# Performance work log

Hardware: AMD Instinct MI355X
Metric: run time of the kernel (lower is better)

The kernel has to match this reference:

```python
import jax, jax.numpy as jnp
import numpy as np

EPS = 1e-5

def _bn(h, gamma, beta):
    # BatchNorm1d in training mode: per-channel stats over the batch dim (L=1)
    m = jnp.mean(h, axis=0)
    v = jnp.var(h, axis=0)  # biased variance, as torch uses for normalization
    return gamma * (h - m) * jax.lax.rsqrt(v + EPS) + beta

def setup_inputs() -> dict:
    key = jax.random.key(0)
    ks = jax.random.split(key, 8)
    vocab, emb = 8192, 512
    inter = (vocab + emb) // 2  # 4352
    N = 8192
    x_t = jax.random.randint(ks[0], (N,), 0, vocab, dtype=jnp.int64)
    W1 = jax.random.normal(ks[1], (inter, vocab), dtype=jnp.float32) * 0.02
    b1 = jax.random.normal(ks[2], (inter,), dtype=jnp.float32) * 0.02
    g1 = jnp.ones((inter,), dtype=jnp.float32)
    beta1 = jnp.zeros((inter,), dtype=jnp.float32)
    W2 = jax.random.normal(ks[3], (emb, inter), dtype=jnp.float32) * 0.02
    b2 = jax.random.normal(ks[4], (emb,), dtype=jnp.float32) * 0.02
    g2 = jnp.ones((emb,), dtype=jnp.float32)
    beta2 = jnp.zeros((emb,), dtype=jnp.float32)
    return {"x_t": x_t, "W1": W1, "b1": b1, "g1": g1, "beta1": beta1,
            "W2": W2, "b2": b2, "g2": g2, "beta2": beta2}

def reference(x_t, W1, b1, g1, beta1, W2, b2, g2, beta2):
    # one_hot(x_t) @ Conv1d(k=1) weight == gather of W1 columns (same math, no dense one-hot)
    h1 = W1.T[x_t] + b1                      # [N, inter]
    h1 = jax.nn.gelu(_bn(h1, g1, beta1), approximate=False)
    h2 = h1 @ W2.T + b2                      # [N, emb]
    out = jax.nn.gelu(_bn(h2, g2, beta2), approximate=False)
    return out
```

## Files before the change

### kernel.cpp

```cpp
#include <hip/hip_runtime.h>
#include <hip/hip_bf16.h>
#include <math.h>

typedef __attribute__((ext_vector_type(8))) short short8;
typedef __attribute__((ext_vector_type(4))) float f32x4;

#define VOCAB 8192
#define NSAMP 8192
#define INTER 4352
#define EMB   512

#define OFF_CNT    0
#define OFF_A1     32768
#define OFF_M1     50176
#define OFF_A2     67584
#define OFF_M2     69632
#define OFF_PS1B   71680
#define OFF_PS2B   1120256
#define OFF_W2B    2168832
#define OFF_HACT   6625280
#define OFF_HPART  77928448
#define PART_BYTES 16777216ULL

__device__ __forceinline__ float gelu_exact(float x) {
    return 0.5f * x * (1.0f + erff(x * 0.70710678118654752f));
}
__device__ __forceinline__ unsigned short f2bf(float x) {
    __hip_bfloat16 b = __float2bfloat16(x);
    return *reinterpret_cast<unsigned short*>(&b);
}
__device__ __forceinline__ void async16(const unsigned short* g, unsigned short* l) {
    __builtin_amdgcn_global_load_lds(
        (const __attribute__((address_space(1))) void*)g,
        (__attribute__((address_space(3))) void*)l, 16, 0, 0);
}

__global__ void k_zero_cnt(int* cnt) {
    cnt[blockIdx.x * 256 + threadIdx.x] = 0;
}
__global__ void k_hist(const int* __restrict__ xt, int* __restrict__ cnt) {
    int n = blockIdx.x * 256 + threadIdx.x;
    atomicAdd(&cnt[xt[n]], 1);
}

__global__ __launch_bounds__(256) void k_stats1(const float* __restrict__ W1,
                                                const int* __restrict__ cnt,
                                                const float* __restrict__ g1,
                                                float* __restrict__ a1,
                                                float* __restrict__ m1) {
    const int t = threadIdx.x, lane = t & 63, w = t >> 6;
    const int row = blockIdx.x * 4 + w;
    const float* wr = W1 + (size_t)row * VOCAB;
    float s1 = 0.f, s2 = 0.f;
    #pragma unroll 8
    for (int it = 0; it < 32; ++it) {
        int v = it * 256 + lane * 4;
        float4 x = *(const float4*)(wr + v);
        int4 c = *(const int4*)(cnt + v);
        float cx = (float)c.x, cy = (float)c.y, cz = (float)c.z, cw = (float)c.w;
        s1 += cx * x.x + cy * x.y + cz * x.z + cw * x.w;
        s2 += cx * x.x * x.x + cy * x.y * x.y + cz * x.z * x.z + cw * x.w * x.w;
    }
    #pragma unroll
    for (int d = 1; d < 64; d <<= 1) {
        s1 += __shfl_xor(s1, d);
        s2 += __shfl_xor(s2, d);
    }
    if (lane == 0) {
        float m = s1 * (1.f / NSAMP);
        float var = s2 * (1.f / NSAMP) - m * m;
        a1[row] = g1[row] * rsqrtf(var + 1e-5f);
        m1[row] = m;
    }
}

__global__ __launch_bounds__(256) void k_build(const float* __restrict__ W1,
                                               const float* __restrict__ a1,
                                               const float* __restrict__ m1,
                                               const float* __restrict__ beta1,
                                               unsigned short* __restrict__ Hact) {
    const int i0 = blockIdx.x * 64;
    const int v0 = blockIdx.y * 256;
    const int t = threadIdx.x;
    const int c0 = (t & 15) * 4;
    const int vg = (t >> 4) * 4;
    float4 av = *(const float4*)(a1 + i0 + c0);
    float4 mv = *(const float4*)(m1 + i0 + c0);
    float4 bv = *(const float4*)(beta1 + i0 + c0);
    const float* ap = (const float*)&av;
    const float* mp = (const float*)&mv;
    const float* bp = (const float*)&bv;
    #pragma unroll
    for (int vi = 0; vi < 4; ++vi) {
        int vb = v0 + vi * 64 + vg;
        float wf[4][4];
        #pragma unroll
        for (int j = 0; j < 4; ++j)
            *(float4*)&wf[j][0] = *(const float4*)(W1 + (size_t)(i0 + c0 + j) * VOCAB + vb);
        #pragma unroll
        for (int k = 0; k < 4; ++k) {
            ushort4 o;
            o.x = f2bf(gelu_exact(ap[0] * (wf[0][k] - mp[0]) + bp[0]));
            o.y = f2bf(gelu_exact(ap[1] * (wf[1][k] - mp[1]) + bp[1]));
            o.z = f2bf(gelu_exact(ap[2] * (wf[2][k] - mp[2]) + bp[2]));
            o.w = f2bf(gelu_exact(ap[3] * (wf[3][k] - mp[3]) + bp[3]));
            *(ushort4*)&Hact[(size_t)(vb + k) * INTER + i0 + c0] = o;
        }
    }
}

__global__ void k_w2bf(const float* __restrict__ W2, unsigned short* __restrict__ W2b) {
    int idx = (blockIdx.x * 256 + threadIdx.x) * 4;
    float4 w = *(const float4*)(W2 + idx);
    ushort4 u;
    u.x = f2bf(w.x); u.y = f2bf(w.y); u.z = f2bf(w.z); u.w = f2bf(w.w);
    *(ushort4*)(W2b + idx) = u;
}

__global__ __launch_bounds__(512) void k_gemm(const unsigned short* __restrict__ A,
                                              const unsigned short* __restrict__ B,
                                              float* __restrict__ Cp, int kPer) {
    __shared__ __align__(16) unsigned short sA[128 * 64];
    __shared__ __align__(16) unsigned short sB[512 * 64];
    const int m0 = blockIdx.x * 128;
    const int kbeg = blockIdx.z * kPer;
    const int kend = kbeg + kPer;
    float* C = Cp + (size_t)blockIdx.z * NSAMP * EMB;
    const int t = threadIdx.x;
    const int lane = t & 63;
    const int wave = t >> 6;
    const int wr = wave >> 2, wc = wave & 3;
    const int mq = lane & 15, kq = lane >> 4;
    const int srow = lane >> 3;
    const int sgrp = lane & 7;
    const int scol = (sgrp ^ srow) * 8;
    const int swz = mq & 7;
    f32x4 acc[4][8];
    #pragma unroll
    for (int r = 0; r < 4; ++r)
        #pragma unroll
        for (int c = 0; c < 8; ++c) acc[r][c] = (f32x4){0.f, 0.f, 0.f, 0.f};
    for (int k0 = kbeg; k0 < kend; k0 += 64) {
        #pragma unroll
        for (int p = 0; p < 2; ++p) {
            int r0 = wave * 16 + p * 8;
            async16(A + (size_t)(m0 + r0 + srow) * INTER + k0 + scol, &sA[r0 * 64]);
        }
        #pragma unroll
        for (int p = 0; p < 8; ++p) {
            int r0 = wave * 64 + p * 8;
            async16(B + (size_t)(r0 + srow) * INTER + k0 + scol, &sB[r0 * 64]);
        }
        __syncthreads();
        #pragma unroll
        for (int kk = 0; kk < 64; kk += 32) {
            const int gbase = kq + (kk >> 3);
            short8 af[4], bf[8];
            #pragma unroll
            for (int r = 0; r < 4; ++r)
                af[r] = *(const short8*)&sA[(wr * 64 + r * 16 + mq) * 64 + ((gbase ^ swz) * 8)];
            #pragma unroll
            for (int c = 0; c < 8; ++c)
                bf[c] = *(const short8*)&sB[(wc * 128 + c * 16 + mq) * 64 + ((gbase ^ swz) * 8)];
            #pragma unroll
            for (int r = 0; r < 4; ++r)
                #pragma unroll
                for (int c = 0; c < 8; ++c)
                    acc[r][c] = __builtin_amdgcn_mfma_f32_16x16x32_bf16(af[r], bf[c], acc[r][c], 0, 0, 0);
        }
        __syncthreads();
    }
    #pragma unroll
    for (int r = 0; r < 4; ++r) {
        #pragma unroll
        for (int c = 0; c < 8; ++c) {
            int col = wc * 128 + c * 16 + mq;
            int rowb = m0 + wr * 64 + r * 16 + kq * 4;
            #pragma unroll
            for (int j = 0; j < 4; ++j)
                C[(size_t)(rowb + j) * EMB + col] = acc[r][c][j];
        }
    }
}

__global__ __launch_bounds__(256) void k_reduce(const float* hpart,
                                                const int* __restrict__ cnt,
                                                float* h2,
                                                float* __restrict__ ps1,
                                                float* __restrict__ ps2, int S) {
    __shared__ float4 b1[128], b2[128];
    const int v0 = blockIdx.x * 16;
    const int t = threadIdx.x;
    const int half = t >> 7;
    const int c4 = (t & 127) * 4;
    float4 acc1 = {0.f, 0.f, 0.f, 0.f}, acc2 = {0.f, 0.f, 0.f, 0.f};
    #pragma unroll
    for (int rp = 0; rp < 8; ++rp) {
        int r = v0 + rp * 2 + half;
        int cw_i = cnt[r];
        if (cw_i > 0) {
            size_t off = (size_t)r * EMB + c4;
            float4 h = *(const float4*)(hpart + off);
            for (int s = 1; s < S; ++s) {
                float4 hs = *(const float4*)(hpart + (size_t)s * NSAMP * EMB + off);
                h.x += hs.x; h.y += hs.y; h.z += hs.z; h.w += hs.w;
            }
            *(float4*)(h2 + off) = h;
            float w = (float)cw_i;
            acc1.x += w * h.x; acc1.y += w * h.y; acc1.z += w * h.z; acc1.w += w * h.w;
            acc2.x += w * h.x * h.x; acc2.y += w * h.y * h.y;
            acc2.z += w * h.z * h.z; acc2.w += w * h.w * h.w;
        }
    }
    if (half == 1) { b1[t & 127] = acc1; b2[t & 127] = acc2; }
    __syncthreads();
    if (half == 0) {
        float4 o1 = b1[t & 127], o2 = b2[t & 127];
        o1.x += acc1.x; o1.y += acc1.y; o1.z += acc1.z; o1.w += acc1.w;
        o2.x += acc2.x; o2.y += acc2.y; o2.z += acc2.z; o2.w += acc2.w;
        ps1[(size_t)(c4 + 0) * 512 + blockIdx.x] = o1.x;
        ps1[(size_t)(c4 + 1) * 512 + blockIdx.x] = o1.y;
        ps1[(size_t)(c4 + 2) * 512 + blockIdx.x] = o1.z;
        ps1[(size_t)(c4 + 3) * 512 + blockIdx.x] = o1.w;
        ps2[(size_t)(c4 + 0) * 512 + blockIdx.x] = o2.x;
        ps2[(size_t)(c4 + 1) * 512 + blockIdx.x] = o2.y;
        ps2[(size_t)(c4 + 2) * 512 + blockIdx.x] = o2.z;
        ps2[(size_t)(c4 + 3) * 512 + blockIdx.x] = o2.w;
    }
}

__global__ __launch_bounds__(256) void k_stats2f(const float* __restrict__ ps1,
                                                 const float* __restrict__ ps2,
                                                 const float* __restrict__ g2,
                                                 float* __restrict__ a2,
                                                 float* __restrict__ m2) {
    const int lane = threadIdx.x & 63;
    const int e = blockIdx.x * 4 + (threadIdx.x >> 6);
    float s1 = 0.f, s2 = 0.f;
    #pragma unroll
    for (int k = 0; k < 8; ++k) {
        s1 += ps1[(size_t)e * 512 + k * 64 + lane];
        s2 += ps2[(size_t)e * 512 + k * 64 + lane];
    }
    #pragma unroll
    for (int d = 1; d < 64; d <<= 1) {
        s1 += __shfl_xor(s1, d);
        s2 += __shfl_xor(s2, d);
    }
    if (lane == 0) {
        float m = s1 * (1.f / NSAMP);
        float var = s2 * (1.f / NSAMP) - m * m;
        a2[e] = g2[e] * rsqrtf(var + 1e-5f);
        m2[e] = m;
    }
}

__global__ __launch_bounds__(256) void k_final(const float* __restrict__ h2,
                                               const int* __restrict__ xt,
                                               const float* __restrict__ a2,
                                               const float* __restrict__ m2,
                                               const float* __restrict__ beta2,
                                               float* __restrict__ out) {
    const int t = threadIdx.x;
    const int n = blockIdx.x * 2 + (t >> 7);
    const int e = (t & 127) * 4;
    const int v = xt[n];
    float4 h = *(const float4*)(h2 + (size_t)v * EMB + e);
    float4 a = *(const float4*)(a2 + e);
    float4 m = *(const float4*)(m2 + e);
    float4 b = *(const float4*)(beta2 + e);
    float4 o;
    o.x = gelu_exact(a.x * (h.x - m.x) + b.x);
    o.y = gelu_exact(a.y * (h.y - m.y) + b.y);
    o.z = gelu_exact(a.z * (h.z - m.z) + b.z);
    o.w = gelu_exact(a.w * (h.w - m.w) + b.w);
    *(float4*)(out + (size_t)n * EMB + e) = o;
}

extern "C" void kernel_launch(void* const* d_in, const int* in_sizes, int n_in,
                              void* d_out, int out_size, void* d_ws, size_t ws_size,
                              hipStream_t stream) {
    const int* xt      = (const int*)d_in[0];
    const float* W1    = (const float*)d_in[1];
    const float* g1    = (const float*)d_in[3];
    const float* beta1 = (const float*)d_in[4];
    const float* W2    = (const float*)d_in[5];
    const float* g2    = (const float*)d_in[7];
    const float* beta2 = (const float*)d_in[8];
    float* out = (float*)d_out;

    char* ws = (char*)d_ws;
    int*   cnt  = (int*)  (ws + OFF_CNT);
    float* a1   = (float*)(ws + OFF_A1);
    float* m1   = (float*)(ws + OFF_M1);
    float* a2   = (float*)(ws + OFF_A2);
    float* m2   = (float*)(ws + OFF_M2);
    float* ps1b = (float*)(ws + OFF_PS1B);
    float* ps2b = (float*)(ws + OFF_PS2B);
    unsigned short* W2b  = (unsigned short*)(ws + OFF_W2B);
    unsigned short* Hact = (unsigned short*)(ws + OFF_HACT);
    float* hpart = (float*)(ws + OFF_HPART);
    float* h2 = hpart;

    int S = 1;
    if (ws_size >= OFF_HPART + 4 * PART_BYTES) S = 4;
    else if (ws_size >= OFF_HPART + 2 * PART_BYTES) S = 2;

    k_zero_cnt<<<32, 256, 0, stream>>>(cnt);
    k_hist<<<32, 256, 0, stream>>>(xt, cnt);
    k_stats1<<<1088, 256, 0, stream>>>(W1, cnt, g1, a1, m1);
    k_build<<<dim3(68, 32), 256, 0, stream>>>(W1, a1, m1, beta1, Hact);
    k_w2bf<<<2176, 256, 0, stream>>>(W2, W2b);
    k_gemm<<<dim3(64, 1, S), 512, 0, stream>>>(Hact, W2b, hpart, INTER / S);
    k_reduce<<<512, 256, 0, stream>>>(hpart, cnt, h2, ps1b, ps2b, S);
    k_stats2f<<<128, 256, 0, stream>>>(ps1b, ps2b, g2, a2, m2);
    k_final<<<4096, 256, 0, stream>>>(h2, xt, a2, m2, beta2, out);
}
```

Measured before the change: 356.3 us.

## Double-buffer GEMM LDS tiles and skip building rows for unused vocab entries

The GEMM main loop moves from a single 64-wide K tile to two 32-wide LDS buffers, issuing the async loads for the next tile before computing on the current one, with one barrier per step. This is meant to overlap global-to-LDS traffic with MFMA work, at the cost of twice as many loop iterations and barriers. k_build now reads the vocab histogram and skips the GELU and bf16 store for vocab rows with zero count. Those rows are presumably never read later, since the GEMM output appears to be indexed per vocab entry. This cuts transcendental work and write bandwidth for vocab entries absent from the input, but leaves stale data in those Hact rows.

New measurement: 369.0 us. 1.04x slower.

```diff
diff --git a/kernel.cpp b/kernel.cpp
--- a/kernel.cpp
+++ b/kernel.cpp
@@ -78,6 +78,7 @@
                                                const float* __restrict__ a1,
                                                const float* __restrict__ m1,
                                                const float* __restrict__ beta1,
+                                               const int* __restrict__ cnt,
                                                unsigned short* __restrict__ Hact) {
     const int i0 = blockIdx.x * 64;
     const int v0 = blockIdx.y * 256;
@@ -93,18 +94,22 @@
     #pragma unroll
     for (int vi = 0; vi < 4; ++vi) {
         int vb = v0 + vi * 64 + vg;
+        int4 cv = *(const int4*)(cnt + vb);
+        const int* cvp = (const int*)&cv;
         float wf[4][4];
         #pragma unroll
         for (int j = 0; j < 4; ++j)
             *(float4*)&wf[j][0] = *(const float4*)(W1 + (size_t)(i0 + c0 + j) * VOCAB + vb);
         #pragma unroll
         for (int k = 0; k < 4; ++k) {
-            ushort4 o;
-            o.x = f2bf(gelu_exact(ap[0] * (wf[0][k] - mp[0]) + bp[0]));
-            o.y = f2bf(gelu_exact(ap[1] * (wf[1][k] - mp[1]) + bp[1]));
-            o.z = f2bf(gelu_exact(ap[2] * (wf[2][k] - mp[2]) + bp[2]));
-            o.w = f2bf(gelu_exact(ap[3] * (wf[3][k] - mp[3]) + bp[3]));
-            *(ushort4*)&Hact[(size_t)(vb + k) * INTER + i0 + c0] = o;
+            if (cvp[k] != 0) {
+                ushort4 o;
+                o.x = f2bf(gelu_exact(ap[0] * (wf[0][k] - mp[0]) + bp[0]));
+                o.y = f2bf(gelu_exact(ap[1] * (wf[1][k] - mp[1]) + bp[1]));
+                o.z = f2bf(gelu_exact(ap[2] * (wf[2][k] - mp[2]) + bp[2]));
+                o.w = f2bf(gelu_exact(ap[3] * (wf[3][k] - mp[3]) + bp[3]));
+                *(ushort4*)&Hact[(size_t)(vb + k) * INTER + i0 + c0] = o;
+            }
         }
     }
 }
@@ -120,8 +125,8 @@
 __global__ __launch_bounds__(512) void k_gemm(const unsigned short* __restrict__ A,
                                               const unsigned short* __restrict__ B,
                                               float* __restrict__ Cp, int kPer) {
-    __shared__ __align__(16) unsigned short sA[128 * 64];
-    __shared__ __align__(16) unsigned short sB[512 * 64];
+    __shared__ __align__(16) unsigned short sA[2][128 * 32];
+    __shared__ __align__(16) unsigned short sB[2][512 * 32];
     const int m0 = blockIdx.x * 128;
     const int kbeg = blockIdx.z * kPer;
     const int kend = kbeg + kPer;
@@ -131,45 +136,52 @@
     const int wave = t >> 6;
     const int wr = wave >> 2, wc = wave & 3;
     const int mq = lane & 15, kq = lane >> 4;
-    const int srow = lane >> 3;
-    const int sgrp = lane & 7;
-    const int scol = (sgrp ^ srow) * 8;
-    const int swz = mq & 7;
+    const int srow = lane >> 2;
+    const int sgrp = lane & 3;
+    const int sf   = (srow & 3) ^ ((srow >> 2) & 3);
+    const int scol = (sgrp ^ sf) * 8;
+    const int rf   = (mq & 3) ^ ((mq >> 2) & 3);
+    const int goff = ((kq ^ rf) * 8);
     f32x4 acc[4][8];
     #pragma unroll
     for (int r = 0; r < 4; ++r)
         #pragma unroll
         for (int c = 0; c < 8; ++c) acc[r][c] = (f32x4){0.f, 0.f, 0.f, 0.f};
-    for (int k0 = kbeg; k0 < kend; k0 += 64) {
-        #pragma unroll
-        for (int p = 0; p < 2; ++p) {
-            int r0 = wave * 16 + p * 8;
-            async16(A + (size_t)(m0 + r0 + srow) * INTER + k0 + scol, &sA[r0 * 64]);
+
+    #define STAGE(buf, kk0)                                                          \
+        {                                                                            \
+            int r0a = wave * 16;                                                     \
+            async16(A + (size_t)(m0 + r0a + srow) * INTER + (kk0) + scol,            \
+                    &sA[buf][r0a * 32]);                                             \
+            _Pragma("unroll")                                                        \
+            for (int p = 0; p < 4; ++p) {                                            \
+                int r0b = wave * 64 + p * 16;                                        \
+                async16(B + (size_t)(r0b + srow) * INTER + (kk0) + scol,             \
+                        &sB[buf][r0b * 32]);                                         \
+            }                                                                        \
         }
-        #pragma unroll
-        for (int p = 0; p < 8; ++p) {
-            int r0 = wave * 64 + p * 8;
-            async16(B + (size_t)(r0 + srow) * INTER + k0 + scol, &sB[r0 * 64]);
-        }
-        __syncthreads();
-        #pragma unroll
-        for (int kk = 0; kk < 64; kk += 32) {
-            const int gbase = kq + (kk >> 3);
-            short8 af[4], bf[8];
-            #pragma unroll
-            for (int r = 0; r < 4; ++r)
-                af[r] = *(const short8*)&sA[(wr * 64 + r * 16 + mq) * 64 + ((gbase ^ swz) * 8)];
+
+    STAGE(0, kbeg);
+    __syncthreads();
+    int cur = 0;
+    for (int k0 = kbeg; k0 < kend; k0 += 32) {
+        if (k0 + 32 < kend) STAGE(cur ^ 1, k0 + 32);
+        short8 af[4], bf[8];
+        #pragma unroll
+        for (int r = 0; r < 4; ++r)
+            af[r] = *(const short8*)&sA[cur][(wr * 64 + r * 16 + mq) * 32 + goff];
+        #pragma unroll
+        for (int c = 0; c < 8; ++c)
+            bf[c] = *(const short8*)&sB[cur][(wc * 128 + c * 16 + mq) * 32 + goff];
+        #pragma unroll
+        for (int r = 0; r < 4; ++r)
             #pragma unroll
             for (int c = 0; c < 8; ++c)
-                bf[c] = *(const short8*)&sB[(wc * 128 + c * 16 + mq) * 64 + ((gbase ^ swz) * 8)];
-            #pragma unroll
-            for (int r = 0; r < 4; ++r)
-                #pragma unroll
-                for (int c = 0; c < 8; ++c)
-                    acc[r][c] = __builtin_amdgcn_mfma_f32_16x16x32_bf16(af[r], bf[c], acc[r][c], 0, 0, 0);
-        }
+                acc[r][c] = __builtin_amdgcn_mfma_f32_16x16x32_bf16(af[r], bf[c], acc[r][c], 0, 0, 0);
         __syncthreads();
-    }
+        cur ^= 1;
+    }
+    #undef STAGE
     #pragma unroll
     for (int r = 0; r < 4; ++r) {
         #pragma unroll
@@ -309,7 +321,7 @@
     k_zero_cnt<<<32, 256, 0, stream>>>(cnt);
     k_hist<<<32, 256, 0, stream>>>(xt, cnt);
     k_stats1<<<1088, 256, 0, stream>>>(W1, cnt, g1, a1, m1);
-    k_build<<<dim3(68, 32), 256, 0, stream>>>(W1, a1, m1, beta1, Hact);
+    k_build<<<dim3(68, 32), 256, 0, stream>>>(W1, a1, m1, beta1, cnt, Hact);
     k_w2bf<<<2176, 256, 0, stream>>>(W2, W2b);
     k_gemm<<<dim3(64, 1, S), 512, 0, stream>>>(Hact, W2b, hpart, INTER / S);
     k_reduce<<<512, 256, 0, stream>>>(hpart, cnt, h2, ps1b, ps2b, S);
```

## Fuse all stages into one persistent kernel with global barriers

Applied to the files above, without the earlier changes.

Replaces the nine separate launches with a single 256-block persistent kernel that runs histogram plus W2 conversion, BN1 stats, Hact build, split-K GEMM, reduce, BN2 stats and the final output as phases separated by atomic-counter grid barriers. It also skips building Hact rows for vocab entries that never occur and fixes split-K at 4. The aim is to remove launch gaps and idle tails between small kernels. The cost is spin-wait barriers, which rely on all 256 blocks being co-resident, and phases that now run at a fixed grid size instead of their natural grid sizes.

Measured after the change: 543.5 us. 52.5% more time.

```diff
diff --git a/kernel.cpp b/kernel.cpp
--- a/kernel.cpp
+++ b/kernel.cpp
@@ -9,18 +9,19 @@
 #define NSAMP 8192
 #define INTER 4352
 #define EMB   512
-
-#define OFF_CNT    0
-#define OFF_A1     32768
-#define OFF_M1     50176
-#define OFF_A2     67584
-#define OFF_M2     69632
-#define OFF_PS1B   71680
-#define OFF_PS2B   1120256
-#define OFF_W2B    2168832
-#define OFF_HACT   6625280
-#define OFF_HPART  77928448
-#define PART_BYTES 16777216ULL
+#define NBLK  256
+
+#define OFF_BAR    0
+#define OFF_CNT    64
+#define OFF_A1     32832
+#define OFF_M1     50240
+#define OFF_A2     67648
+#define OFF_M2     69696
+#define OFF_PS1B   71744
+#define OFF_PS2B   596032
+#define OFF_W2B    1120320
+#define OFF_HACT   5576768
+#define OFF_HPART  76879936
 
 __device__ __forceinline__ float gelu_exact(float x) {
     return 0.5f * x * (1.0f + erff(x * 0.70710678118654752f));
@@ -35,246 +36,292 @@
         (__attribute__((address_space(3))) void*)l, 16, 0, 0);
 }
 
-__global__ void k_zero_cnt(int* cnt) {
-    cnt[blockIdx.x * 256 + threadIdx.x] = 0;
-}
-__global__ void k_hist(const int* __restrict__ xt, int* __restrict__ cnt) {
-    int n = blockIdx.x * 256 + threadIdx.x;
-    atomicAdd(&cnt[xt[n]], 1);
-}
-
-__global__ __launch_bounds__(256) void k_stats1(const float* __restrict__ W1,
-                                                const int* __restrict__ cnt,
-                                                const float* __restrict__ g1,
-                                                float* __restrict__ a1,
-                                                float* __restrict__ m1) {
-    const int t = threadIdx.x, lane = t & 63, w = t >> 6;
-    const int row = blockIdx.x * 4 + w;
-    const float* wr = W1 + (size_t)row * VOCAB;
-    float s1 = 0.f, s2 = 0.f;
-    #pragma unroll 8
-    for (int it = 0; it < 32; ++it) {
-        int v = it * 256 + lane * 4;
-        float4 x = *(const float4*)(wr + v);
-        int4 c = *(const int4*)(cnt + v);
-        float cx = (float)c.x, cy = (float)c.y, cz = (float)c.z, cw = (float)c.w;
-        s1 += cx * x.x + cy * x.y + cz * x.z + cw * x.w;
-        s2 += cx * x.x * x.x + cy * x.y * x.y + cz * x.z * x.z + cw * x.w * x.w;
-    }
-    #pragma unroll
-    for (int d = 1; d < 64; d <<= 1) {
-        s1 += __shfl_xor(s1, d);
-        s2 += __shfl_xor(s2, d);
-    }
-    if (lane == 0) {
-        float m = s1 * (1.f / NSAMP);
-        float var = s2 * (1.f / NSAMP) - m * m;
-        a1[row] = g1[row] * rsqrtf(var + 1e-5f);
-        m1[row] = m;
-    }
-}
-
-__global__ __launch_bounds__(256) void k_build(const float* __restrict__ W1,
-                                               const float* __restrict__ a1,
-                                               const float* __restrict__ m1,
-                                               const float* __restrict__ beta1,
-                                               unsigned short* __restrict__ Hact) {
-    const int i0 = blockIdx.x * 64;
-    const int v0 = blockIdx.y * 256;
-    const int t = threadIdx.x;
-    const int c0 = (t & 15) * 4;
-    const int vg = (t >> 4) * 4;
-    float4 av = *(const float4*)(a1 + i0 + c0);
-    float4 mv = *(const float4*)(m1 + i0 + c0);
-    float4 bv = *(const float4*)(beta1 + i0 + c0);
-    const float* ap = (const float*)&av;
-    const float* mp = (const float*)&mv;
-    const float* bp = (const float*)&bv;
-    #pragma unroll
-    for (int vi = 0; vi < 4; ++vi) {
-        int vb = v0 + vi * 64 + vg;
-        float wf[4][4];
-        #pragma unroll
-        for (int j = 0; j < 4; ++j)
-            *(float4*)&wf[j][0] = *(const float4*)(W1 + (size_t)(i0 + c0 + j) * VOCAB + vb);
-        #pragma unroll
-        for (int k = 0; k < 4; ++k) {
-            ushort4 o;
-            o.x = f2bf(gelu_exact(ap[0] * (wf[0][k] - mp[0]) + bp[0]));
-            o.y = f2bf(gelu_exact(ap[1] * (wf[1][k] - mp[1]) + bp[1]));
-            o.z = f2bf(gelu_exact(ap[2] * (wf[2][k] - mp[2]) + bp[2]));
-            o.w = f2bf(gelu_exact(ap[3] * (wf[3][k] - mp[3]) + bp[3]));
-            *(ushort4*)&Hact[(size_t)(vb + k) * INTER + i0 + c0] = o;
-        }
-    }
-}
-
-__global__ void k_w2bf(const float* __restrict__ W2, unsigned short* __restrict__ W2b) {
-    int idx = (blockIdx.x * 256 + threadIdx.x) * 4;
-    float4 w = *(const float4*)(W2 + idx);
-    ushort4 u;
-    u.x = f2bf(w.x); u.y = f2bf(w.y); u.z = f2bf(w.z); u.w = f2bf(w.w);
-    *(ushort4*)(W2b + idx) = u;
-}
-
-__global__ __launch_bounds__(512) void k_gemm(const unsigned short* __restrict__ A,
-                                              const unsigned short* __restrict__ B,
-                                              float* __restrict__ Cp, int kPer) {
-    __shared__ __align__(16) unsigned short sA[128 * 64];
-    __shared__ __align__(16) unsigned short sB[512 * 64];
-    const int m0 = blockIdx.x * 128;
-    const int kbeg = blockIdx.z * kPer;
-    const int kend = kbeg + kPer;
-    float* C = Cp + (size_t)blockIdx.z * NSAMP * EMB;
+__device__ __forceinline__ void gbar(int* bar, int target) {
+    __syncthreads();
+    if (threadIdx.x == 0) {
+        __threadfence();
+        atomicAdd(bar, 1);
+        while (atomicAdd(bar, 0) < target) __builtin_amdgcn_s_sleep(2);
+        __threadfence();
+    }
+    __syncthreads();
+}
+
+__global__ __launch_bounds__(512, 2) void k_mega(const int* __restrict__ xt,
+                                                 const float* __restrict__ W1,
+                                                 const float* __restrict__ g1,
+                                                 const float* __restrict__ beta1,
+                                                 const float* __restrict__ W2,
+                                                 const float* __restrict__ g2,
+                                                 const float* __restrict__ beta2,
+                                                 float* __restrict__ out,
+                                                 char* ws) {
+    __shared__ __align__(16) unsigned char lds[81920];
+    int*   bar  = (int*)  (ws + OFF_BAR);
+    int*   cnt  = (int*)  (ws + OFF_CNT);
+    float* a1   = (float*)(ws + OFF_A1);
+    float* m1   = (float*)(ws + OFF_M1);
+    float* a2   = (float*)(ws + OFF_A2);
+    float* m2   = (float*)(ws + OFF_M2);
+    float* ps1  = (float*)(ws + OFF_PS1B);
+    float* ps2  = (float*)(ws + OFF_PS2B);
+    unsigned short* W2b  = (unsigned short*)(ws + OFF_W2B);
+    unsigned short* Hact = (unsigned short*)(ws + OFF_HACT);
+    float* hpart = (float*)(ws + OFF_HPART);
+    float* h2 = hpart;
+
+    const int blk = blockIdx.x;
     const int t = threadIdx.x;
     const int lane = t & 63;
-    const int wave = t >> 6;
-    const int wr = wave >> 2, wc = wave & 3;
-    const int mq = lane & 15, kq = lane >> 4;
-    const int srow = lane >> 3;
-    const int sgrp = lane & 7;
-    const int scol = (sgrp ^ srow) * 8;
-    const int swz = mq & 7;
-    f32x4 acc[4][8];
-    #pragma unroll
-    for (int r = 0; r < 4; ++r)
-        #pragma unroll
-        for (int c = 0; c < 8; ++c) acc[r][c] = (f32x4){0.f, 0.f, 0.f, 0.f};
-    for (int k0 = kbeg; k0 < kend; k0 += 64) {
-        #pragma unroll
-        for (int p = 0; p < 2; ++p) {
-            int r0 = wave * 16 + p * 8;
-            async16(A + (size_t)(m0 + r0 + srow) * INTER + k0 + scol, &sA[r0 * 64]);
-        }
-        #pragma unroll
-        for (int p = 0; p < 8; ++p) {
-            int r0 = wave * 64 + p * 8;
-            async16(B + (size_t)(r0 + srow) * INTER + k0 + scol, &sB[r0 * 64]);
-        }
+    const int wv = t >> 6;
+
+    if (blk < 16) {
+        int n = blk * 512 + t;
+        atomicAdd(&cnt[xt[n]], 1);
+    } else {
+        const int bw = blk - 16;
+        #pragma unroll
+        for (int it = 0; it < 5; ++it) {
+            int i = (it * 240 + bw) * 512 + t;
+            if (i < 557056) {
+                float4 w = *(const float4*)(W2 + (size_t)i * 4);
+                ushort4 u;
+                u.x = f2bf(w.x); u.y = f2bf(w.y); u.z = f2bf(w.z); u.w = f2bf(w.w);
+                *(ushort4*)(W2b + (size_t)i * 4) = u;
+            }
+        }
+    }
+    gbar(bar, NBLK * 1);
+
+    {
+        float* cntf = (float*)lds;
+        for (int i = t; i < VOCAB; i += 512) cntf[i] = (float)cnt[i];
         __syncthreads();
         #pragma unroll
-        for (int kk = 0; kk < 64; kk += 32) {
-            const int gbase = kq + (kk >> 3);
-            short8 af[4], bf[8];
-            #pragma unroll
-            for (int r = 0; r < 4; ++r)
-                af[r] = *(const short8*)&sA[(wr * 64 + r * 16 + mq) * 64 + ((gbase ^ swz) * 8)];
-            #pragma unroll
-            for (int c = 0; c < 8; ++c)
-                bf[c] = *(const short8*)&sB[(wc * 128 + c * 16 + mq) * 64 + ((gbase ^ swz) * 8)];
-            #pragma unroll
-            for (int r = 0; r < 4; ++r)
+        for (int rep = 0; rep < 3; ++rep) {
+            int row = blk * 8 + wv + rep * 2048;
+            if (row < INTER) {
+                const float* wr = W1 + (size_t)row * VOCAB;
+                float s1 = 0.f, s2 = 0.f;
+                #pragma unroll 4
+                for (int it = 0; it < 32; ++it) {
+                    int v = it * 256 + lane * 4;
+                    float4 x = *(const float4*)(wr + v);
+                    float4 c = *(const float4*)(cntf + v);
+                    s1 += c.x * x.x + c.y * x.y + c.z * x.z + c.w * x.w;
+                    s2 += c.x * x.x * x.x + c.y * x.y * x.y + c.z * x.z * x.z + c.w * x.w * x.w;
+                }
+                #pragma unroll
+                for (int d = 1; d < 64; d <<= 1) {
+                    s1 += __shfl_xor(s1, d);
+                    s2 += __shfl_xor(s2, d);
+                }
+                if (lane == 0) {
+                    float m = s1 * (1.f / NSAMP);
+                    float var = s2 * (1.f / NSAMP) - m * m;
+                    a1[row] = g1[row] * rsqrtf(var + 1e-5f);
+                    m1[row] = m;
+                }
+            }
+        }
+    }
+    gbar(bar, NBLK * 2);
+
+    {
+        const int c0 = (t & 15) * 4;
+        const int vg = (t >> 4) * 4;
+        #pragma unroll
+        for (int it = 0; it < 5; ++it) {
+            int tix = it * 256 + blk;
+            if (tix < 1088) {
+                int i0 = (tix % 68) * 64;
+                int v0 = (tix / 68) * 512;
+                float4 av = *(const float4*)(a1 + i0 + c0);
+                float4 mv = *(const float4*)(m1 + i0 + c0);
+                float4 bv = *(const float4*)(beta1 + i0 + c0);
+                const float* ap = (const float*)&av;
+                const float* mp = (const float*)&mv;
+                const float* bp = (const float*)&bv;
+                #pragma unroll
+                for (int vi = 0; vi < 4; ++vi) {
+                    int vb = v0 + vi * 128 + vg;
+                    int4 cv = *(const int4*)(cnt + vb);
+                    const int* cvp = (const int*)&cv;
+                    float wf[4][4];
+                    #pragma unroll
+                    for (int j = 0; j < 4; ++j)
+                        *(float4*)&wf[j][0] = *(const float4*)(W1 + (size_t)(i0 + c0 + j) * VOCAB + vb);
+                    #pragma unroll
+                    for (int k = 0; k < 4; ++k) {
+                        if (cvp[k] != 0) {
+                            ushort4 o;
+                            o.x = f2bf(gelu_exact(ap[0] * (wf[0][k] - mp[0]) + bp[0]));
+                            o.y = f2bf(gelu_exact(ap[1] * (wf[1][k] - mp[1]) + bp[1]));
+                            o.z = f2bf(gelu_exact(ap[2] * (wf[2][k] - mp[2]) + bp[2]));
+                            o.w = f2bf(gelu_exact(ap[3] * (wf[3][k] - mp[3]) + bp[3]));
+                            *(ushort4*)&Hact[(size_t)(vb + k) * INTER + i0 + c0] = o;
+                        }
+                    }
+                }
+            }
+        }
+    }
+    gbar(bar, NBLK * 3);
+
+    {
+        unsigned short* sA = (unsigned short*)lds;
+        unsigned short* sB = (unsigned short*)(lds + 16384);
+        const int m0 = (blk & 63) * 128;
+        const int z  = blk >> 6;
+        const int kbeg = z * 1088;
+        float* C = hpart + (size_t)z * (NSAMP * EMB);
+        const int wave = wv;
+        const int wr = wave >> 2, wc = wave & 3;
+        const int mq = lane & 15, kq = lane >> 4;
+        const int srow = lane >> 3;
+        const int sgrp = lane & 7;
+        const int scol = (sgrp ^ srow) * 8;
+        const int swz = mq & 7;
+        f32x4 acc[4][8];
+        #pragma unroll
+        for (int r = 0; r < 4; ++r)
+            #pragma unroll
+            for (int c = 0; c < 8; ++c) acc[r][c] = (f32x4){0.f, 0.f, 0.f, 0.f};
+        for (int k0 = kbeg; k0 < kbeg + 1088; k0 += 64) {
+            #pragma unroll
+            for (int p = 0; p < 2; ++p) {
+                int r0 = wave * 16 + p * 8;
+                async16(Hact + (size_t)(m0 + r0 + srow) * INTER + k0 + scol, sA + r0 * 64);
+            }
+            #pragma unroll
+            for (int p = 0; p < 8; ++p) {
+                int r0 = wave * 64 + p * 8;
+                async16(W2b + (size_t)(r0 + srow) * INTER + k0 + scol, sB + r0 * 64);
+            }
+            __syncthreads();
+            #pragma unroll
+            for (int kk = 0; kk < 64; kk += 32) {
+                const int gbase = kq + (kk >> 3);
+                short8 af[4], bf[8];
+                #pragma unroll
+                for (int r = 0; r < 4; ++r)
+                    af[r] = *(const short8*)&sA[(wr * 64 + r * 16 + mq) * 64 + ((gbase ^ swz) * 8)];
                 #pragma unroll
                 for (int c = 0; c < 8; ++c)
-                    acc[r][c] = __builtin_amdgcn_mfma_f32_16x16x32_bf16(af[r], bf[c], acc[r][c], 0, 0, 0);
-        }
+                    bf[c] = *(const short8*)&sB[(wc * 128 + c * 16 + mq) * 64 + ((gbase ^ swz) * 8)];
+                #pragma unroll
+                for (int r = 0; r < 4; ++r)
+                    #pragma unroll
+                    for (int c = 0; c < 8; ++c)
+                        acc[r][c] = __builtin_amdgcn_mfma_f32_16x16x32_bf16(af[r], bf[c], acc[r][c], 0, 0, 0);
+            }
+            __syncthreads();
+        }
+        #pragma unroll
+        for (int r = 0; r < 4; ++r) {
+            #pragma unroll
+            for (int c = 0; c < 8; ++c) {
+                int col = wc * 128 + c * 16 + mq;
+                int rowb = m0 + wr * 64 + r * 16 + kq * 4;
+                #pragma unroll
+                for (int j = 0; j < 4; ++j)
+                    C[(size_t)(rowb + j) * EMB + col] = acc[r][c][j];
+            }
+        }
+    }
+    gbar(bar, NBLK * 4);
+
+    {
+        const int v0 = blk * 32;
+        const int g = t >> 7;
+        const int c4 = (t & 127) * 4;
+        float4 s1v = {0.f,0.f,0.f,0.f}, s2v = {0.f,0.f,0.f,0.f};
+        #pragma unroll
+        for (int rp = 0; rp < 8; ++rp) {
+            int r = v0 + rp * 4 + g;
+            int cw = cnt[r];
+            if (cw > 0) {
+                size_t off = (size_t)r * EMB + c4;
+                float4 h = *(const float4*)(hpart + off);
+                #pragma unroll
+                for (int s = 1; s < 4; ++s) {
+                    float4 hs = *(const float4*)(hpart + (size_t)s * (NSAMP * EMB) + off);
+                    h.x += hs.x; h.y += hs.y; h.z += hs.z; h.w += hs.w;
+                }
+                *(float4*)(h2 + off) = h;
+                float w = (float)cw;
+                s1v.x += w * h.x; s1v.y += w * h.y; s1v.z += w * h.z; s1v.w += w * h.w;
+                s2v.x += w * h.x * h.x; s2v.y += w * h.y * h.y;
+                s2v.z += w * h.z * h.z; s2v.w += w * h.w * h.w;
+            }
+        }
+        float4* r1 = (float4*)lds;
+        float4* r2 = r1 + 384;
         __syncthreads();
-    }
-    #pragma unroll
-    for (int r = 0; r < 4; ++r) {
-        #pragma unroll
-        for (int c = 0; c < 8; ++c) {
-            int col = wc * 128 + c * 16 + mq;
-            int rowb = m0 + wr * 64 + r * 16 + kq * 4;
-            #pragma unroll
-            for (int j = 0; j < 4; ++j)
-                C[(size_t)(rowb + j) * EMB + col] = acc[r][c][j];
-        }
-    }
-}
-
-__global__ __launch_bounds__(256) void k_reduce(const float* hpart,
-                                                const int* __restrict__ cnt,
-                                                float* h2,
-                                                float* __restrict__ ps1,
-                                                float* __restrict__ ps2, int S) {
-    __shared__ float4 b1[128], b2[128];
-    const int v0 = blockIdx.x * 16;
-    const int t = threadIdx.x;
-    const int half = t >> 7;
-    const int c4 = (t & 127) * 4;
-    float4 acc1 = {0.f, 0.f, 0.f, 0.f}, acc2 = {0.f, 0.f, 0.f, 0.f};
-    #pragma unroll
-    for (int rp = 0; rp < 8; ++rp) {
-        int r = v0 + rp * 2 + half;
-        int cw_i = cnt[r];
-        if (cw_i > 0) {
-            size_t off = (size_t)r * EMB + c4;
-            float4 h = *(const float4*)(hpart + off);
-            for (int s = 1; s < S; ++s) {
-                float4 hs = *(const float4*)(hpart + (size_t)s * NSAMP * EMB + off);
-                h.x += hs.x; h.y += hs.y; h.z += hs.z; h.w += hs.w;
-            }
-            *(float4*)(h2 + off) = h;
-            float w = (float)cw_i;
-            acc1.x += w * h.x; acc1.y += w * h.y; acc1.z += w * h.z; acc1.w += w * h.w;
-            acc2.x += w * h.x * h.x; acc2.y += w * h.y * h.y;
-            acc2.z += w * h.z * h.z; acc2.w += w * h.w * h.w;
-        }
-    }
-    if (half == 1) { b1[t & 127] = acc1; b2[t & 127] = acc2; }
-    __syncthreads();
-    if (half == 0) {
-        float4 o1 = b1[t & 127], o2 = b2[t & 127];
-        o1.x += acc1.x; o1.y += acc1.y; o1.z += acc1.z; o1.w += acc1.w;
-        o2.x += acc2.x; o2.y += acc2.y; o2.z += acc2.z; o2.w += acc2.w;
-        ps1[(size_t)(c4 + 0) * 512 + blockIdx.x] = o1.x;
-        ps1[(size_t)(c4 + 1) * 512 + blockIdx.x] = o1.y;
-        ps1[(size_t)(c4 + 2) * 512 + blockIdx.x] = o1.z;
-        ps1[(size_t)(c4 + 3) * 512 + blockIdx.x] = o1.w;
-        ps2[(size_t)(c4 + 0) * 512 + blockIdx.x] = o2.x;
-        ps2[(size_t)(c4 + 1) * 512 + blockIdx.x] = o2.y;
-        ps2[(size_t)(c4 + 2) * 512 + blockIdx.x] = o2.z;
-        ps2[(size_t)(c4 + 3) * 512 + blockIdx.x] = o2.w;
-    }
-}
-
-__global__ __launch_bounds__(256) void k_stats2f(const float* __restrict__ ps1,
-                                                 const float* __restrict__ ps2,
-                                                 const float* __restrict__ g2,
-                                                 float* __restrict__ a2,
-                                                 float* __restrict__ m2) {
-    const int lane = threadIdx.x & 63;
-    const int e = blockIdx.x * 4 + (threadIdx.x >> 6);
-    float s1 = 0.f, s2 = 0.f;
-    #pragma unroll
-    for (int k = 0; k < 8; ++k) {
-        s1 += ps1[(size_t)e * 512 + k * 64 + lane];
-        s2 += ps2[(size_t)e * 512 + k * 64 + lane];
-    }
-    #pragma unroll
-    for (int d = 1; d < 64; d <<= 1) {
-        s1 += __shfl_xor(s1, d);
-        s2 += __shfl_xor(s2, d);
-    }
-    if (lane == 0) {
-        float m = s1 * (1.f / NSAMP);
-        float var = s2 * (1.f / NSAMP) - m * m;
-        a2[e] = g2[e] * rsqrtf(var + 1e-5f);
-        m2[e] = m;
-    }
-}
-
-__global__ __launch_bounds__(256) void k_final(const float* __restrict__ h2,
-                                               const int* __restrict__ xt,
-                                               const float* __restrict__ a2,
-                                               const float* __restrict__ m2,
-                                               const float* __restrict__ beta2,
-                                               float* __restrict__ out) {
-    const int t = threadIdx.x;
-    const int n = blockIdx.x * 2 + (t >> 7);
-    const int e = (t & 127) * 4;
-    const int v = xt[n];
-    float4 h = *(const float4*)(h2 + (size_t)v * EMB + e);
-    float4 a = *(const float4*)(a2 + e);
-    float4 m = *(const float4*)(m2 + e);
-    float4 b = *(const float4*)(beta2 + e);
-    float4 o;
-    o.x = gelu_exact(a.x * (h.x - m.x) + b.x);
-    o.y = gelu_exact(a.y * (h.y - m.y) + b.y);
-    o.z = gelu_exact(a.z * (h.z - m.z) + b.z);
-    o.w = gelu_exact(a.w * (h.w - m.w) + b.w);
-    *(float4*)(out + (size_t)n * EMB + e) = o;
+        if (g > 0) { r1[(g - 1) * 128 + (t & 127)] = s1v; r2[(g - 1) * 128 + (t & 127)] = s2v; }
+        __syncthreads();
+        if (g == 0) {
+            #pragma unroll
+            for (int q = 0; q < 3; ++q) {
+                float4 x = r1[q * 128 + (t & 127)], y = r2[q * 128 + (t & 127)];
+                s1v.x += x.x; s1v.y += x.y; s1v.z += x.z; s1v.w += x.w;
+                s2v.x += y.x; s2v.y += y.y; s2v.z += y.z; s2v.w += y.w;
+            }
+            ps1[(size_t)(c4 + 0) * 256 + blk] = s1v.x;
+            ps1[(size_t)(c4 + 1) * 256 + blk] = s1v.y;
+            ps1[(size_t)(c4 + 2) * 256 + blk] = s1v.z;
+            ps1[(size_t)(c4 + 3) * 256 + blk] = s1v.w;
+            ps2[(size_t)(c4 + 0) * 256 + blk] = s2v.x;
+            ps2[(size_t)(c4 + 1) * 256 + blk] = s2v.y;
+            ps2[(size_t)(c4 + 2) * 256 + blk] = s2v.z;
+            ps2[(size_t)(c4 + 3) * 256 + blk] = s2v.w;
+        }
+    }
+    gbar(bar, NBLK * 5);
+
+    {
+        int e = blk * 8 + wv;
+        if (e < EMB) {
+            float s1 = 0.f, s2 = 0.f;
+            #pragma unroll
+            for (int q = 0; q < 4; ++q) {
+                s1 += ps1[(size_t)e * 256 + q * 64 + lane];
+                s2 += ps2[(size_t)e * 256 + q * 64 + lane];
+            }
+            #pragma unroll
+            for (int d = 1; d < 64; d <<= 1) {
+                s1 += __shfl_xor(s1, d);
+                s2 += __shfl_xor(s2, d);
+            }
+            if (lane == 0) {
+                float m = s1 * (1.f / NSAMP);
+                float var = s2 * (1.f / NSAMP) - m * m;
+                a2[e] = g2[e] * rsqrtf(var + 1e-5f);
+                m2[e] = m;
+            }
+        }
+    }
+    gbar(bar, NBLK * 6);
+
+    {
+        #pragma unroll
+        for (int it = 0; it < 8; ++it) {
+            int idx = it * 131072 + blk * 512 + t;
+            int n = idx >> 7;
+            int e = (idx & 127) * 4;
+            int v = xt[n];
+            float4 h = *(const float4*)(h2 + (size_t)v * EMB + e);
+            float4 a = *(const float4*)(a2 + e);
+            float4 m = *(const float4*)(m2 + e);
+            float4 b = *(const float4*)(beta2 + e);
+            float4 o;
+            o.x = gelu_exact(a.x * (h.x - m.x) + b.x);
+            o.y = gelu_exact(a.y * (h.y - m.y) + b.y);
+            o.z = gelu_exact(a.z * (h.z - m.z) + b.z);
+            o.w = gelu_exact(a.w * (h.w - m.w) + b.w);
+            *(float4*)(out + (size_t)idx * 4) = o;
+        }
+    }
 }
 
 extern "C" void kernel_launch(void* const* d_in, const int* in_sizes, int n_in,
@@ -289,30 +336,6 @@
     const float* beta2 = (const float*)d_in[8];
     float* out = (float*)d_out;
 
-    char* ws = (char*)d_ws;
-    int*   cnt  = (int*)  (ws + OFF_CNT);
-    float* a1   = (float*)(ws + OFF_A1);
-    float* m1   = (float*)(ws + OFF_M1);
-    float* a2   = (float*)(ws + OFF_A2);
-    float* m2   = (float*)(ws + OFF_M2);
-    float* ps1b = (float*)(ws + OFF_PS1B);
-    float* ps2b = (float*)(ws + OFF_PS2B);
-    unsigned short* W2b  = (unsigned short*)(ws + OFF_W2B);
-    unsigned short* Hact = (unsigned short*)(ws + OFF_HACT);
-    float* hpart = (float*)(ws + OFF_HPART);
-    float* h2 = hpart;
-
-    int S = 1;
-    if (ws_size >= OFF_HPART + 4 * PART_BYTES) S = 4;
-    else if (ws_size >= OFF_HPART + 2 * PART_BYTES) S = 2;
-
-    k_zero_cnt<<<32, 256, 0, stream>>>(cnt);
-    k_hist<<<32, 256, 0, stream>>>(xt, cnt);
-    k_stats1<<<1088, 256, 0, stream>>>(W1, cnt, g1, a1, m1);
-    k_build<<<dim3(68, 32), 256, 0, stream>>>(W1, a1, m1, beta1, Hact);
-    k_w2bf<<<2176, 256, 0, stream>>>(W2, W2b);
-    k_gemm<<<dim3(64, 1, S), 512, 0, stream>>>(Hact, W2b, hpart, INTER / S);
-    k_reduce<<<512, 256, 0, stream>>>(hpart, cnt, h2, ps1b, ps2b, S);
-    k_stats2f<<<128, 256, 0, stream>>>(ps1b, ps2b, g2, a2, m2);
-    k_final<<<4096, 256, 0, stream>>>(h2, xt, a2, m2, beta2, out);
-}
+    hipMemsetAsync(d_ws, 0, 32832, stream);
+    k_mega<<<NBLK, 512, 0, stream>>>(xt, W1, g1, beta1, W2, g2, beta2, out, (char*)d_ws);
+}
```

## Skip Hact rows for unused vocab, stage counts in LDS, flatten gemm grid

Applied to the files above, without the earlier changes.

k_build now reads the token histogram and writes a GELU row only for vocabulary entries that actually occur. Unused rows stay uninitialized, and the gemm presumably relies on their zero counts in the reduce step, which is a risk if garbage values such as NaN leak through. k_stats1 converts the count vector to float once in shared memory per block instead of reloading it per iteration. The zeroing kernel is replaced with hipMemsetAsync, and the gemm grid is flattened so that split-K blocks for the same M tile are interleaved.

Result: slower. 367.8 us (+3.2%).

```diff
diff --git a/kernel.cpp b/kernel.cpp
--- a/kernel.cpp
+++ b/kernel.cpp
@@ -35,9 +35,6 @@
         (__attribute__((address_space(3))) void*)l, 16, 0, 0);
 }
 
-__global__ void k_zero_cnt(int* cnt) {
-    cnt[blockIdx.x * 256 + threadIdx.x] = 0;
-}
 __global__ void k_hist(const int* __restrict__ xt, int* __restrict__ cnt) {
     int n = blockIdx.x * 256 + threadIdx.x;
     atomicAdd(&cnt[xt[n]], 1);
@@ -48,7 +45,10 @@
                                                 const float* __restrict__ g1,
                                                 float* __restrict__ a1,
                                                 float* __restrict__ m1) {
+    __shared__ __align__(16) float cntf[VOCAB];
     const int t = threadIdx.x, lane = t & 63, w = t >> 6;
+    for (int i = t; i < VOCAB; i += 256) cntf[i] = (float)cnt[i];
+    __syncthreads();
     const int row = blockIdx.x * 4 + w;
     const float* wr = W1 + (size_t)row * VOCAB;
     float s1 = 0.f, s2 = 0.f;
@@ -56,10 +56,9 @@
     for (int it = 0; it < 32; ++it) {
         int v = it * 256 + lane * 4;
         float4 x = *(const float4*)(wr + v);
-        int4 c = *(const int4*)(cnt + v);
-        float cx = (float)c.x, cy = (float)c.y, cz = (float)c.z, cw = (float)c.w;
-        s1 += cx * x.x + cy * x.y + cz * x.z + cw * x.w;
-        s2 += cx * x.x * x.x + cy * x.y * x.y + cz * x.z * x.z + cw * x.w * x.w;
+        float4 c = *(const float4*)(cntf + v);
+        s1 += c.x * x.x + c.y * x.y + c.z * x.z + c.w * x.w;
+        s2 += c.x * x.x * x.x + c.y * x.y * x.y + c.z * x.z * x.z + c.w * x.w * x.w;
     }
     #pragma unroll
     for (int d = 1; d < 64; d <<= 1) {
@@ -78,6 +77,7 @@
                                                const float* __restrict__ a1,
                                                const float* __restrict__ m1,
                                                const float* __restrict__ beta1,
+                                               const int* __restrict__ cnt,
                                                unsigned short* __restrict__ Hact) {
     const int i0 = blockIdx.x * 64;
     const int v0 = blockIdx.y * 256;
@@ -93,18 +93,22 @@
     #pragma unroll
     for (int vi = 0; vi < 4; ++vi) {
         int vb = v0 + vi * 64 + vg;
+        int4 cv = *(const int4*)(cnt + vb);
+        const int* cvp = (const int*)&cv;
         float wf[4][4];
         #pragma unroll
         for (int j = 0; j < 4; ++j)
             *(float4*)&wf[j][0] = *(const float4*)(W1 + (size_t)(i0 + c0 + j) * VOCAB + vb);
         #pragma unroll
         for (int k = 0; k < 4; ++k) {
-            ushort4 o;
-            o.x = f2bf(gelu_exact(ap[0] * (wf[0][k] - mp[0]) + bp[0]));
-            o.y = f2bf(gelu_exact(ap[1] * (wf[1][k] - mp[1]) + bp[1]));
-            o.z = f2bf(gelu_exact(ap[2] * (wf[2][k] - mp[2]) + bp[2]));
-            o.w = f2bf(gelu_exact(ap[3] * (wf[3][k] - mp[3]) + bp[3]));
-            *(ushort4*)&Hact[(size_t)(vb + k) * INTER + i0 + c0] = o;
+            if (cvp[k] != 0) {
+                ushort4 o;
+                o.x = f2bf(gelu_exact(ap[0] * (wf[0][k] - mp[0]) + bp[0]));
+                o.y = f2bf(gelu_exact(ap[1] * (wf[1][k] - mp[1]) + bp[1]));
+                o.z = f2bf(gelu_exact(ap[2] * (wf[2][k] - mp[2]) + bp[2]));
+                o.w = f2bf(gelu_exact(ap[3] * (wf[3][k] - mp[3]) + bp[3]));
+                *(ushort4*)&Hact[(size_t)(vb + k) * INTER + i0 + c0] = o;
+            }
         }
     }
 }
@@ -119,13 +123,15 @@
 
 __global__ __launch_bounds__(512) void k_gemm(const unsigned short* __restrict__ A,
                                               const unsigned short* __restrict__ B,
-                                              float* __restrict__ Cp, int kPer) {
+                                              float* __restrict__ Cp, int kPer, int S) {
     __shared__ __align__(16) unsigned short sA[128 * 64];
     __shared__ __align__(16) unsigned short sB[512 * 64];
-    const int m0 = blockIdx.x * 128;
-    const int kbeg = blockIdx.z * kPer;
+    const int blk = blockIdx.x;
+    const int z = blk & (S - 1);
+    const int m0 = (blk / S) * 128;
+    const int kbeg = z * kPer;
     const int kend = kbeg + kPer;
-    float* C = Cp + (size_t)blockIdx.z * NSAMP * EMB;
+    float* C = Cp + (size_t)z * (NSAMP * EMB);
     const int t = threadIdx.x;
     const int lane = t & 63;
     const int wave = t >> 6;
@@ -306,12 +312,12 @@
     if (ws_size >= OFF_HPART + 4 * PART_BYTES) S = 4;
     else if (ws_size >= OFF_HPART + 2 * PART_BYTES) S = 2;
 
-    k_zero_cnt<<<32, 256, 0, stream>>>(cnt);
+    hipMemsetAsync(cnt, 0, 32768, stream);
     k_hist<<<32, 256, 0, stream>>>(xt, cnt);
     k_stats1<<<1088, 256, 0, stream>>>(W1, cnt, g1, a1, m1);
-    k_build<<<dim3(68, 32), 256, 0, stream>>>(W1, a1, m1, beta1, Hact);
+    k_build<<<dim3(68, 32), 256, 0, stream>>>(W1, a1, m1, beta1, cnt, Hact);
     k_w2bf<<<2176, 256, 0, stream>>>(W2, W2b);
-    k_gemm<<<dim3(64, 1, S), 512, 0, stream>>>(Hact, W2b, hpart, INTER / S);
+    k_gemm<<<64 * S, 512, 0, stream>>>(Hact, W2b, hpart, INTER / S, S);
     k_reduce<<<512, 256, 0, stream>>>(hpart, cnt, h2, ps1b, ps2b, S);
     k_stats2f<<<128, 256, 0, stream>>>(ps1b, ps2b, g2, a2, m2);
     k_final<<<4096, 256, 0, stream>>>(h2, xt, a2, m2, beta2, out);
```
